# Kernel optimization log

Measured on AMD Instinct MI355X. Metric: run time of the kernel, lower is better.

Reference implementation:

```python
import jax, jax.numpy as jnp
import numpy as np

VISUAL_WEIGHT = 0.01

def setup_inputs() -> dict:
    key = jax.random.key(0)
    ks = jax.random.split(key, 10)
    h = w = 96
    inp = {
        'feat_src': jax.random.normal(ks[0], (1, 256, h, w), jnp.float32),
        'feat_ref': jax.random.normal(ks[1], (1, 256, h, w), jnp.float32),
        'landmarks_src': jax.random.normal(ks[2], (1, 136, h, w), jnp.float32),
        'landmarks_ref': jax.random.normal(ks[3], (1, 136, h, w), jnp.float32),
        'mask_src': jax.random.randint(ks[4], (1, 1, h, w), 0, 3, jnp.int32),
        'mask_ref': jax.random.randint(ks[5], (1, 1, h, w), 0, 3, jnp.int32),
        'conv1_w': jax.random.normal(ks[6], (256,), jnp.float32) * 0.05,
        'conv1_b': jax.random.normal(ks[7], (1,), jnp.float32) * 0.05,
        'conv2_w': jax.random.normal(ks[8], (256,), jnp.float32) * 0.05,
        'conv2_b': jax.random.normal(ks[9], (1,), jnp.float32) * 0.05,
    }
    return inp

def reference(feat_src, feat_ref, landmarks_src, landmarks_ref, mask_src, mask_ref,
              conv1_w, conv1_b, conv2_w, conv2_b):
    b, c, h, w = feat_src.shape  # b == 1 assumed by original code
    hw = h * w
    ck = c + 136
    # 1x1 convs (256 -> 1): einsum over channel
    beta = jnp.einsum('bchw,c->bhw', feat_ref, conv1_w) + conv1_b[:, None, None]  # (1,h,w)
    gama = jnp.einsum('bchw,c->bhw', feat_ref, conv2_w) + conv2_b[:, None, None]
    # concat visual features with landmark heatmaps, then RAW reshape (as in torch)
    src = jnp.concatenate([VISUAL_WEIGHT * feat_src, landmarks_src], axis=1)  # (1,392,h,w)
    ref = jnp.concatenate([VISUAL_WEIGHT * feat_ref, landmarks_ref], axis=1)
    feat_lm_src = jnp.reshape(src, (hw, ck))   # raw reshape, faithful to torch
    feat_lm_ref = jnp.reshape(ref, (ck, hw))
    # element-wise mask equality -> (hw,) vector, broadcast over columns of A
    M = (jnp.reshape(mask_src, (hw,)) == jnp.reshape(mask_ref, (hw,))).astype(feat_src.dtype)
    A = feat_lm_src @ feat_lm_ref            # (hw, hw)
    A = jax.nn.softmax(A, axis=0)
    A = A * M                                 # broadcast on last dim, same as torch
    beta_hat = jnp.reshape(A @ jnp.reshape(beta, (hw, 1)), (1, h, w))
    gama_hat = jnp.reshape(A @ jnp.reshape(gama, (hw, 1)), (1, h, w))
    # gama_hat.expand((1,1,h,w)) * feat_src + beta_hat
    feat_src_trans = gama_hat[None] * feat_src + beta_hat[None]
    return feat_src_trans
```

## Files before the change

### kernel.cpp

```cpp
#include <hip/hip_runtime.h>

#define HW    9216
#define CK    392
#define NVIS  2359296
#define KP    672
#define NKT   21
#define NKT_SHORT 13
#define BM_SPLIT 47
#define NRB   144
#define MAXN  3584
#define NB_N  28
#define PSRC_BLOCKS 3024

typedef __bf16 bf16_t;
typedef __bf16 bf16x8 __attribute__((ext_vector_type(8)));
typedef __bf16 bf16x4v __attribute__((ext_vector_type(4)));
typedef unsigned short ushort8v __attribute__((ext_vector_type(8)));
typedef float  f32x4  __attribute__((ext_vector_type(4)));

typedef __attribute__((address_space(1))) void void_g;
typedef __attribute__((address_space(3))) void void_l;

static __device__ __forceinline__ void gload16(const void* g, void* l) {
  __builtin_amdgcn_global_load_lds((const void_g*)g, (void_l*)l, 16, 0, 0);
}

__global__ __launch_bounds__(256) void fused_prep(
    const float* __restrict__ feat_src, const float* __restrict__ lm_src,
    const float* __restrict__ fr, const int* __restrict__ ms,
    const int* __restrict__ mr, const float* __restrict__ w1,
    const float* __restrict__ b1, const float* __restrict__ w2,
    const float* __restrict__ b2,
    bf16_t* __restrict__ Sp, int* __restrict__ sel,
    float* __restrict__ wbs, float* __restrict__ wgs, int* __restrict__ cnt)
{
  __shared__ float r1[4][64], r2[4][64];
  __shared__ int sb[4], st[4];
  int bid = blockIdx.x, t = threadIdx.x;

  if (bid < PSRC_BLOCKS) {
    int tid = bid * 256 + t;
    int i = tid / 84, kc = tid - i * 84;
    int ko = kc * 8;
    int j0 = 0; bool lo = false, zero = false;
    if (kc < 49)       j0 = ko;
    else if (kc < 66)  j0 = ko - 136;
    else if (kc < 83) { j0 = ko - 272; lo = true; }
    else               zero = true;
    bf16x8 pk = {};
    if (!zero) {
      int idx0 = i * CK + j0;
      const float* src = (idx0 < NVIS) ? (feat_src + idx0) : (lm_src + (idx0 - NVIS));
      float sc = (idx0 < NVIS) ? 0.01f : 1.f;
      float4 v0 = *reinterpret_cast<const float4*>(src);
      float4 v1 = *reinterpret_cast<const float4*>(src + 4);
      float x[8] = {v0.x, v0.y, v0.z, v0.w, v1.x, v1.y, v1.z, v1.w};
      #pragma unroll
      for (int e = 0; e < 8; ++e) {
        float xv = sc * x[e];
        bf16_t h = (bf16_t)xv;
        pk[e] = lo ? (bf16_t)(xv - (float)h) : h;
      }
    }
    *reinterpret_cast<bf16x8*>(Sp + (long)tid * 8) = pk;
  } else {
    int b = bid - PSRC_BLOCKS;
    int qi = t & 63, cg = t >> 6, lane = t & 63, wid = t >> 6;
    int q0 = b * 64;
    float a1 = 0.f, a2 = 0.f;
    #pragma unroll 4
    for (int c = cg * 64; c < cg * 64 + 64; ++c) {
      float v = fr[(long)c * HW + q0 + qi];
      a1 += v * w1[c]; a2 += v * w2[c];
    }
    r1[cg][qi] = a1; r2[cg][qi] = a2;
    int cb = 0, ct = 0;
    for (int q = t; q < HW; q += 256) {
      bool f = (ms[q] == mr[q]);
      ct += f ? 1 : 0;
      cb += (f && q < q0) ? 1 : 0;
    }
    #pragma unroll
    for (int d = 1; d < 64; d <<= 1) {
      cb += __shfl_xor(cb, d);
      ct += __shfl_xor(ct, d);
    }
    if (lane == 0) { sb[wid] = cb; st[wid] = ct; }
    __syncthreads();
    int base = sb[0] + sb[1] + sb[2] + sb[3];
    if (t == 0 && b == 0) cnt[0] = st[0] + st[1] + st[2] + st[3];
    if (wid == 0) {
      int q = q0 + lane;
      bool flag = (ms[q] == mr[q]);
      unsigned long long mk = __ballot(flag);
      int pos = __popcll(mk & ((1ull << lane) - 1ull));
      if (flag) {
        int idx = base + pos;
        sel[idx] = q;
        wbs[idx] = r1[0][lane] + r1[1][lane] + r1[2][lane] + r1[3][lane] + b1[0];
        wgs[idx] = r2[0][lane] + r2[1][lane] + r2[2][lane] + r2[3][lane] + b2[0];
      }
    }
  }
}

__global__ __launch_bounds__(256) void prep_ref(
    const float* __restrict__ feat_ref, const float* __restrict__ lm_ref,
    const int* __restrict__ sel, const int* __restrict__ cnt,
    bf16_t* __restrict__ Rp)
{
  int nsel = cnt[0];
  int n128 = (nsel + 127) & ~127;
  int qt = blockIdx.y;
  if (qt * 32 >= n128) return;
  __shared__ bf16_t tile[32][33];
  int x = threadIdx.x & 31, y = threadIdx.x >> 5;
  int kt = blockIdx.x;
  int n = qt * 32 + x;
  int q = (n < nsel) ? sel[n] : -1;
  #pragma unroll
  for (int ry = 0; ry < 4; ++ry) {
    int kl = y + ry * 8;
    int k = kt * 32 + kl;
    int j = -1; bool lo = false;
    if (k < 392)      j = k;
    else if (k < 528) { j = k - 136; lo = true; }
    else if (k < 664) j = k - 272;
    bf16_t v = (bf16_t)0.f;
    if (j >= 0 && q >= 0) {
      int idx = j * HW + q;
      float xv = (idx < NVIS) ? 0.01f * feat_ref[idx] : lm_ref[idx - NVIS];
      bf16_t h = (bf16_t)xv;
      v = lo ? (bf16_t)(xv - (float)h) : h;
    }
    tile[kl][x] = v;
  }
  __syncthreads();
  #pragma unroll
  for (int ry = 0; ry < 4; ++ry) {
    int ql = y + ry * 8;
    int k = kt * 32 + x;
    Rp[(long)(qt * 32 + ql) * KP + k] = tile[x][ql];
  }
}

__global__ __launch_bounds__(256, 2) void gemm_e(
    const bf16_t* __restrict__ Sp, const bf16_t* __restrict__ Rp,
    const int* __restrict__ cnt, bf16_t* __restrict__ E, float* __restrict__ pd)
{
  const int bm = blockIdx.x, bn = blockIdx.y;
  if (bn * 128 >= ((cnt[0] + 127) & ~127)) return;
  __shared__ __align__(16) bf16_t As[128 * 32];
  __shared__ __align__(16) bf16_t Bs[128 * 32];
  const int t = threadIdx.x, w = t >> 6, lane = t & 63;
  const int wr = w >> 1, wc = w & 1;
  const int nkt = (bm < BM_SPLIT) ? NKT_SHORT : NKT;
  f32x4 acc[4][4] = {};

  const int chs = ((lane & 3) ^ ((lane >> 3) & 3)) * 8;
  const bf16_t* sA = Sp + (long)(bm * 128 + w * 32 + (lane >> 2)) * KP + chs;
  const bf16_t* sB = Rp + (long)(bn * 128 + w * 32 + (lane >> 2)) * KP + chs;
  bf16_t* lA = As + w * 1024;
  bf16_t* lB = Bs + w * 1024;
  const int sub = lane >> 4, r16 = lane & 15;
  const int swz = (sub ^ ((r16 >> 1) & 3)) * 8;
  const int aoff = (wr * 64 + r16) * 32 + swz;
  const int boff = (wc * 64 + r16) * 32 + swz;

  for (int kt = 0; kt < nkt; ++kt) {
    gload16(sA, lA);
    gload16(sA + 16 * KP, lA + 512);
    gload16(sB, lB);
    gload16(sB + 16 * KP, lB + 512);
    sA += 32; sB += 32;
    __syncthreads();
    bf16x8 a[4], b[4];
    #pragma unroll
    for (int m = 0; m < 4; ++m)
      a[m] = *reinterpret_cast<const bf16x8*>(As + aoff + m * 512);
    #pragma unroll
    for (int n = 0; n < 4; ++n)
      b[n] = *reinterpret_cast<const bf16x8*>(Bs + boff + n * 512);
    #pragma unroll
    for (int m = 0; m < 4; ++m)
      #pragma unroll
      for (int n = 0; n < 4; ++n)
        acc[m][n] = __builtin_amdgcn_mfma_f32_16x16x32_bf16(a[m], b[n], acc[m][n], 0, 0, 0);
    __syncthreads();
  }

  #pragma unroll
  for (int m = 0; m < 4; ++m)
    #pragma unroll
    for (int n = 0; n < 4; ++n)
      #pragma unroll
      for (int r = 0; r < 4; ++r)
        acc[m][n][r] = __expf(acc[m][n][r]);

  const int C = bn * 128 + wc * 64;
  {
    const int rb = bm * 2 + wr;
    float s[4];
    #pragma unroll
    for (int n = 0; n < 4; ++n) {
      float v = 0.f;
      #pragma unroll
      for (int m = 0; m < 4; ++m)
        #pragma unroll
        for (int r = 0; r < 4; ++r) v += acc[m][n][r];
      v += __shfl_xor(v, 16);
      v += __shfl_xor(v, 32);
      s[n] = v;
    }
    if (sub == 0) {
      f32x4 sv = {s[0], s[1], s[2], s[3]};
      *reinterpret_cast<f32x4*>(pd + (long)rb * MAXN + C + r16 * 4) = sv;
    }
  }
  bf16_t* Eb = E + (long)(bm * 128 + wr * 64 + sub * 4) * MAXN + C + r16 * 4;
  #pragma unroll
  for (int m = 0; m < 4; ++m)
    #pragma unroll
    for (int r = 0; r < 4; ++r) {
      bf16x4v pk;
      #pragma unroll
      for (int n = 0; n < 4; ++n) pk[n] = (bf16_t)acc[m][n][r];
      *reinterpret_cast<bf16x4v*>(Eb + (long)(m * 16 + r) * MAXN) = pk;
    }
}

__global__ __launch_bounds__(256) void make_u(
    const float* __restrict__ pd, const float* __restrict__ wbs,
    const float* __restrict__ wgs, const int* __restrict__ cnt,
    float* __restrict__ ub, float* __restrict__ ug)
{
  __shared__ float sD[4][64];
  int t = threadIdx.x, c = t & 63, g = t >> 6;
  int p = blockIdx.x * 64 + c;
  float D = 0.f;
  for (int rb = g * 36; rb < g * 36 + 36; ++rb)
    D += pd[(long)rb * MAXN + p];
  sD[g][c] = D;
  __syncthreads();
  if (g == 0) {
    int nsel = cnt[0];
    int n128 = (nsel + 127) & ~127;
    float Dt = sD[0][c] + sD[1][c] + sD[2][c] + sD[3][c];
    float vb = 0.f, vg = 0.f;
    if (p < n128) {
      int orig = (p & ~63) + (p & 3) * 16 + ((p >> 2) & 15);
      if (orig < nsel) {
        float inv = 1.f / Dt;
        vb = wbs[orig] * inv;
        vg = wgs[orig] * inv;
      }
    }
    ub[p] = vb;
    ug[p] = vg;
  }
}

__global__ __launch_bounds__(256) void matvec_fin(
    const bf16_t* __restrict__ E, const float* __restrict__ ub,
    const float* __restrict__ ug, const int* __restrict__ cnt,
    const float* __restrict__ fs, float* __restrict__ out)
{
  __shared__ float bhs[16], ghs[16];
  int t = threadIdx.x, lane = t & 63, wv = t >> 6;
  int n128 = (cnt[0] + 127) & ~127;
  int R0 = blockIdx.x * 16;
  const bf16_t* Ew = E + (long)(R0 + wv * 4) * MAXN;
  float ab[4] = {}, ag[4] = {};
  for (int base = 0; base < n128; base += 512) {
    int c0 = base + lane * 8;
    if (c0 < n128) {
      float4 u0a = *reinterpret_cast<const float4*>(ub + c0);
      float4 u0b = *reinterpret_cast<const float4*>(ub + c0 + 4);
      float4 u1a = *reinterpret_cast<const float4*>(ug + c0);
      float4 u1b = *reinterpret_cast<const float4*>(ug + c0 + 4);
      float u0[8] = {u0a.x, u0a.y, u0a.z, u0a.w, u0b.x, u0b.y, u0b.z, u0b.w};
      float u1[8] = {u1a.x, u1a.y, u1a.z, u1a.w, u1b.x, u1b.y, u1b.z, u1b.w};
      #pragma unroll
      for (int rr = 0; rr < 4; ++rr) {
        ushort8v e = *reinterpret_cast<const ushort8v*>(Ew + (long)rr * MAXN + c0);
        #pragma unroll
        for (int j = 0; j < 8; ++j) {
          float ev = __uint_as_float(((unsigned)e[j]) << 16);
          ab[rr] += ev * u0[j];
          ag[rr] += ev * u1[j];
        }
      }
    }
  }
  #pragma unroll
  for (int rr = 0; rr < 4; ++rr) {
    #pragma unroll
    for (int d = 1; d < 64; d <<= 1) {
      ab[rr] += __shfl_xor(ab[rr], d);
      ag[rr] += __shfl_xor(ag[rr], d);
    }
    if (lane == 0) { bhs[wv * 4 + rr] = ab[rr]; ghs[wv * 4 + rr] = ag[rr]; }
  }
  __syncthreads();
  int p = t & 15, cg = t >> 4;
  int P = R0 + p;
  float bv = bhs[p], gv = ghs[p];
  #pragma unroll 4
  for (int c = cg; c < 256; c += 16)
    out[(long)c * HW + P] = gv * fs[(long)c * HW + P] + bv;
}

extern "C" void kernel_launch(void* const* d_in, const int* in_sizes, int n_in,
                              void* d_out, int out_size, void* d_ws, size_t ws_size,
                              hipStream_t stream) {
  const float* feat_src = (const float*)d_in[0];
  const float* feat_ref = (const float*)d_in[1];
  const float* lm_src   = (const float*)d_in[2];
  const float* lm_ref   = (const float*)d_in[3];
  const int*   mask_src = (const int*)d_in[4];
  const int*   mask_ref = (const int*)d_in[5];
  const float* w1 = (const float*)d_in[6];
  const float* b1 = (const float*)d_in[7];
  const float* w2 = (const float*)d_in[8];
  const float* b2 = (const float*)d_in[9];
  float* out = (float*)d_out;

  char* ws = (char*)d_ws;
  bf16_t* Sp   = (bf16_t*)(ws);
  bf16_t* Rp   = (bf16_t*)(ws + 12386304);
  bf16_t* E    = (bf16_t*)(ws + 17203200);
  float* pd    = (float*)(ws + 83263488);
  float* wb    = (float*)(ws + 85327872);
  float* wg    = (float*)(ws + 85342208);
  float* ub    = (float*)(ws + 85356544);
  float* ug    = (float*)(ws + 85370880);
  int*   sel   = (int*)  (ws + 85385216);
  int*   cnt   = (int*)  (ws + 85399552);

  fused_prep<<<PSRC_BLOCKS + HW / 64, 256, 0, stream>>>(
      feat_src, lm_src, feat_ref, mask_src, mask_ref, w1, b1, w2, b2,
      Sp, sel, wb, wg, cnt);
  prep_ref<<<dim3(NKT, MAXN / 32), 256, 0, stream>>>(feat_ref, lm_ref, sel, cnt, Rp);
  gemm_e<<<dim3(72, NB_N), 256, 0, stream>>>(Sp, Rp, cnt, E, pd);
  make_u<<<MAXN / 64, 256, 0, stream>>>(pd, wb, wg, cnt, ub, ug);
  matvec_fin<<<HW / 16, 256, 0, stream>>>(E, ub, ug, cnt, feat_src, out);
}
```

Baseline: 174.8 us.

## Accumulate softmax denominators with atomics and drop the make_u kernel

```diff
diff --git a/kernel.cpp b/kernel.cpp
--- a/kernel.cpp
+++ b/kernel.cpp
@@ -7,7 +7,6 @@
 #define NKT   21
 #define NKT_SHORT 13
 #define BM_SPLIT 47
-#define NRB   144
 #define MAXN  3584
 #define NB_N  28
 #define PSRC_BLOCKS 3024
@@ -32,7 +31,8 @@
     const float* __restrict__ b1, const float* __restrict__ w2,
     const float* __restrict__ b2,
     bf16_t* __restrict__ Sp, int* __restrict__ sel,
-    float* __restrict__ wbs, float* __restrict__ wgs, int* __restrict__ cnt)
+    float* __restrict__ wbs, float* __restrict__ wgs,
+    float* __restrict__ Dg, int* __restrict__ cnt)
 {
   __shared__ float r1[4][64], r2[4][64];
   __shared__ int sb[4], st[4];
@@ -88,7 +88,8 @@
     if (lane == 0) { sb[wid] = cb; st[wid] = ct; }
     __syncthreads();
     int base = sb[0] + sb[1] + sb[2] + sb[3];
-    if (t == 0 && b == 0) cnt[0] = st[0] + st[1] + st[2] + st[3];
+    int nsel = st[0] + st[1] + st[2] + st[3];
+    if (t == 0 && b == 0) cnt[0] = nsel;
     if (wid == 0) {
       int q = q0 + lane;
       bool flag = (ms[q] == mr[q]);
@@ -97,9 +98,18 @@
       if (flag) {
         int idx = base + pos;
         sel[idx] = q;
-        wbs[idx] = r1[0][lane] + r1[1][lane] + r1[2][lane] + r1[3][lane] + b1[0];
-        wgs[idx] = r2[0][lane] + r2[1][lane] + r2[2][lane] + r2[3][lane] + b2[0];
+        int pkx = (idx & ~63) | ((idx & 15) << 2) | ((idx >> 4) & 3);
+        wbs[pkx] = r1[0][lane] + r1[1][lane] + r1[2][lane] + r1[3][lane] + b1[0];
+        wgs[pkx] = r2[0][lane] + r2[1][lane] + r2[2][lane] + r2[3][lane] + b2[0];
       }
+    }
+    if (b == 0) {
+      int n128 = (nsel + 127) & ~127;
+      for (int p = (nsel & ~63) + t; p < n128; p += 256) {
+        int orig = (p & ~63) + (p & 3) * 16 + ((p >> 2) & 15);
+        if (orig >= nsel) { wbs[p] = 0.f; wgs[p] = 0.f; }
+      }
+      for (int i = t; i < MAXN; i += 256) Dg[i] = 0.f;
     }
   }
 }
@@ -146,7 +156,7 @@
 
 __global__ __launch_bounds__(256, 2) void gemm_e(
     const bf16_t* __restrict__ Sp, const bf16_t* __restrict__ Rp,
-    const int* __restrict__ cnt, bf16_t* __restrict__ E, float* __restrict__ pd)
+    const int* __restrict__ cnt, bf16_t* __restrict__ E, float* __restrict__ Dg)
 {
   const int bm = blockIdx.x, bn = blockIdx.y;
   if (bn * 128 >= ((cnt[0] + 127) & ~127)) return;
@@ -199,7 +209,6 @@
 
   const int C = bn * 128 + wc * 64;
   {
-    const int rb = bm * 2 + wr;
     float s[4];
     #pragma unroll
     for (int n = 0; n < 4; ++n) {
@@ -213,8 +222,9 @@
       s[n] = v;
     }
     if (sub == 0) {
-      f32x4 sv = {s[0], s[1], s[2], s[3]};
-      *reinterpret_cast<f32x4*>(pd + (long)rb * MAXN + C + r16 * 4) = sv;
+      #pragma unroll
+      for (int n = 0; n < 4; ++n)
+        atomicAdd(&Dg[C + r16 * 4 + n], s[n]);
     }
   }
   bf16_t* Eb = E + (long)(bm * 128 + wr * 64 + sub * 4) * MAXN + C + r16 * 4;
@@ -229,41 +239,11 @@
     }
 }
 
-__global__ __launch_bounds__(256) void make_u(
-    const float* __restrict__ pd, const float* __restrict__ wbs,
-    const float* __restrict__ wgs, const int* __restrict__ cnt,
-    float* __restrict__ ub, float* __restrict__ ug)
-{
-  __shared__ float sD[4][64];
-  int t = threadIdx.x, c = t & 63, g = t >> 6;
-  int p = blockIdx.x * 64 + c;
-  float D = 0.f;
-  for (int rb = g * 36; rb < g * 36 + 36; ++rb)
-    D += pd[(long)rb * MAXN + p];
-  sD[g][c] = D;
-  __syncthreads();
-  if (g == 0) {
-    int nsel = cnt[0];
-    int n128 = (nsel + 127) & ~127;
-    float Dt = sD[0][c] + sD[1][c] + sD[2][c] + sD[3][c];
-    float vb = 0.f, vg = 0.f;
-    if (p < n128) {
-      int orig = (p & ~63) + (p & 3) * 16 + ((p >> 2) & 15);
-      if (orig < nsel) {
-        float inv = 1.f / Dt;
-        vb = wbs[orig] * inv;
-        vg = wgs[orig] * inv;
-      }
-    }
-    ub[p] = vb;
-    ug[p] = vg;
-  }
-}
-
 __global__ __launch_bounds__(256) void matvec_fin(
-    const bf16_t* __restrict__ E, const float* __restrict__ ub,
-    const float* __restrict__ ug, const int* __restrict__ cnt,
-    const float* __restrict__ fs, float* __restrict__ out)
+    const bf16_t* __restrict__ E, const float* __restrict__ wb,
+    const float* __restrict__ wg, const float* __restrict__ Dg,
+    const int* __restrict__ cnt, const float* __restrict__ fs,
+    float* __restrict__ out)
 {
   __shared__ float bhs[16], ghs[16];
   int t = threadIdx.x, lane = t & 63, wv = t >> 6;
@@ -274,12 +254,21 @@
   for (int base = 0; base < n128; base += 512) {
     int c0 = base + lane * 8;
     if (c0 < n128) {
-      float4 u0a = *reinterpret_cast<const float4*>(ub + c0);
-      float4 u0b = *reinterpret_cast<const float4*>(ub + c0 + 4);
-      float4 u1a = *reinterpret_cast<const float4*>(ug + c0);
-      float4 u1b = *reinterpret_cast<const float4*>(ug + c0 + 4);
-      float u0[8] = {u0a.x, u0a.y, u0a.z, u0a.w, u0b.x, u0b.y, u0b.z, u0b.w};
-      float u1[8] = {u1a.x, u1a.y, u1a.z, u1a.w, u1b.x, u1b.y, u1b.z, u1b.w};
+      float4 b0 = *reinterpret_cast<const float4*>(wb + c0);
+      float4 b1 = *reinterpret_cast<const float4*>(wb + c0 + 4);
+      float4 g0 = *reinterpret_cast<const float4*>(wg + c0);
+      float4 g1 = *reinterpret_cast<const float4*>(wg + c0 + 4);
+      float4 d0 = *reinterpret_cast<const float4*>(Dg + c0);
+      float4 d1 = *reinterpret_cast<const float4*>(Dg + c0 + 4);
+      float u0[8], u1[8];
+      float rc[8] = {__builtin_amdgcn_rcpf(d0.x), __builtin_amdgcn_rcpf(d0.y),
+                     __builtin_amdgcn_rcpf(d0.z), __builtin_amdgcn_rcpf(d0.w),
+                     __builtin_amdgcn_rcpf(d1.x), __builtin_amdgcn_rcpf(d1.y),
+                     __builtin_amdgcn_rcpf(d1.z), __builtin_amdgcn_rcpf(d1.w)};
+      float bb[8] = {b0.x, b0.y, b0.z, b0.w, b1.x, b1.y, b1.z, b1.w};
+      float gg[8] = {g0.x, g0.y, g0.z, g0.w, g1.x, g1.y, g1.z, g1.w};
+      #pragma unroll
+      for (int j = 0; j < 8; ++j) { u0[j] = bb[j] * rc[j]; u1[j] = gg[j] * rc[j]; }
       #pragma unroll
       for (int rr = 0; rr < 4; ++rr) {
         ushort8v e = *reinterpret_cast<const ushort8v*>(Ew + (long)rr * MAXN + c0);
@@ -329,19 +318,16 @@
   bf16_t* Sp   = (bf16_t*)(ws);
   bf16_t* Rp   = (bf16_t*)(ws + 12386304);
   bf16_t* E    = (bf16_t*)(ws + 17203200);
-  float* pd    = (float*)(ws + 83263488);
-  float* wb    = (float*)(ws + 85327872);
-  float* wg    = (float*)(ws + 85342208);
-  float* ub    = (float*)(ws + 85356544);
-  float* ug    = (float*)(ws + 85370880);
-  int*   sel   = (int*)  (ws + 85385216);
-  int*   cnt   = (int*)  (ws + 85399552);
+  float* wb    = (float*)(ws + 83263488);
+  float* wg    = (float*)(ws + 83277824);
+  float* Dg    = (float*)(ws + 83292160);
+  int*   sel   = (int*)  (ws + 83306496);
+  int*   cnt   = (int*)  (ws + 83322880);
 
   fused_prep<<<PSRC_BLOCKS + HW / 64, 256, 0, stream>>>(
       feat_src, lm_src, feat_ref, mask_src, mask_ref, w1, b1, w2, b2,
-      Sp, sel, wb, wg, cnt);
+      Sp, sel, wb, wg, Dg, cnt);
   prep_ref<<<dim3(NKT, MAXN / 32), 256, 0, stream>>>(feat_ref, lm_ref, sel, cnt, Rp);
-  gemm_e<<<dim3(72, NB_N), 256, 0, stream>>>(Sp, Rp, cnt, E, pd);
-  make_u<<<MAXN / 64, 256, 0, stream>>>(pd, wb, wg, cnt, ub, ug);
-  matvec_fin<<<HW / 16, 256, 0, stream>>>(E, ub, ug, cnt, feat_src, out);
-}
+  gemm_e<<<dim3(72, NB_N), 256, 0, stream>>>(Sp, Rp, cnt, E, Dg);
+  matvec_fin<<<HW / 16, 256, 0, stream>>>(E, wb, wg, Dg, cnt, feat_src, out);
+}
```

New measurement: 188.5 us. 1.08x slower.
